# Kernel tuning notes

Measured on AMD Instinct MI355X. Metric: run time of the kernel, lower is better.

Reference implementation:

```python
import jax, jax.numpy as jnp
import numpy as np

EMBED_DIM = 1024
PROJ_DIM = 256


def setup_inputs() -> dict:
    key = jax.random.key(0)
    kx, kq, kk = jax.random.split(key, 3)
    x = jax.random.normal(kx, (8, 4096, EMBED_DIM), dtype=jnp.float32)
    scale = 1.0 / (PROJ_DIM ** 0.5)
    q_proj = jax.random.normal(kq, (EMBED_DIM, PROJ_DIM), dtype=jnp.float32) * scale
    k_proj = jax.random.normal(kk, (EMBED_DIM, PROJ_DIM), dtype=jnp.float32) * scale
    return {"x": x, "q_proj": q_proj, "k_proj": k_proj}


def reference(x, q_proj, k_proj):
    # exp feature maps (FAVOR-style)
    q_prime = jnp.exp(jnp.einsum('bld,de->ble', x, q_proj))  # [B, L, E]
    k_prime = jnp.exp(jnp.einsum('bld,de->ble', x, k_proj))  # [B, L, E]
    # associative KV summary: O(L*E*D)
    kv = jnp.einsum('ble,bld->bed', k_prime, x)               # [B, E, D]
    num = jnp.einsum('ble,bed->bld', q_prime, kv)             # [B, L, D]
    z = 1.0 / (jnp.sum(q_prime, axis=-1, keepdims=True) + 1e-8)
    return num * z
```

## Files before the change

kernel.cpp:

```cpp
#include <hip/hip_runtime.h>


#define EMBED 1024
#define PROJ  256
#define LSEQ  4096
#define BATCH 8

typedef short  bfrag __attribute__((ext_vector_type(8)));
typedef float  f4    __attribute__((ext_vector_type(4)));
typedef unsigned short u16x8 __attribute__((ext_vector_type(8)));
typedef unsigned short u16x4 __attribute__((ext_vector_type(4)));

static __device__ __forceinline__ unsigned short f2bf(float f) {
  unsigned int u = __builtin_bit_cast(unsigned int, f);
  u += 0x7fffu + ((u >> 16) & 1u);
  return (unsigned short)(u >> 16);
}
static __device__ __forceinline__ float bf2f(unsigned short h) {
  unsigned int u = ((unsigned int)h) << 16;
  return __builtin_bit_cast(float, u);
}

static __device__ __forceinline__ void gload_lds16(const void* g, void* l) {
  __builtin_amdgcn_global_load_lds(
      (__attribute__((address_space(1))) void*)(unsigned long long)(g),
      (__attribute__((address_space(3))) void*)(unsigned)(unsigned long long)(l),
      16, 0, 0);
}

static __device__ __forceinline__ void stage_tile(
    const unsigned short* __restrict__ src, int row0, int stride, int k0,
    unsigned short* lds, int wave, int lane) {
#pragma unroll
  for (int j = 0; j < 4; j++) {
    int slot = (wave * 4 + j) * 64 + lane;
    int r = slot >> 3, cp = slot & 7;
    int c = cp ^ (r & 7);
    gload_lds16(src + (size_t)(row0 + r) * stride + k0 + c * 8,
                lds + (wave * 4 + j) * 512);
  }
}

static __device__ __forceinline__ void stage_tile_blk(
    const unsigned short* __restrict__ src, int row0, int ntcols, int k0,
    unsigned short* lds, int wave, int lane) {
#pragma unroll
  for (int j = 0; j < 4; j++) {
    int slot = (wave * 4 + j) * 64 + lane;
    int r = slot >> 3, cp = slot & 7;
    int c = cp ^ (r & 7);
    const unsigned short* blob =
        src + ((((size_t)(row0 >> 6) + (r >> 6)) * ntcols + (k0 >> 6)) << 12);
    gload_lds16(blob + ((r & 63) << 6) + c * 8, lds + (wave * 4 + j) * 512);
  }
}

static __device__ __forceinline__ bfrag read_frag(const unsigned short* lds,
                                                  int row, int chunk) {
  return *(const bfrag*)(lds + ((row << 3) + (chunk ^ (row & 7))) * 8);
}

__global__ __launch_bounds__(256) void cvtb_kernel(
    const float* __restrict__ x, unsigned short* __restrict__ xb) {
  const size_t total = (size_t)BATCH * LSEQ * EMBED;
  size_t i = ((size_t)blockIdx.x * 256 + threadIdx.x) * 8;
  const size_t stride = (size_t)gridDim.x * 256 * 8;
  for (; i < total; i += stride) {
    f4 a = *(const f4*)(x + i);
    f4 b = *(const f4*)(x + i + 4);
    u16x8 h = (u16x8){f2bf(a[0]), f2bf(a[1]), f2bf(a[2]), f2bf(a[3]),
                      f2bf(b[0]), f2bf(b[1]), f2bf(b[2]), f2bf(b[3])};
    *(u16x8*)(xb + i) = h;
  }
}

__global__ __launch_bounds__(256) void cvtw_kernel(
    const float* __restrict__ qw, const float* __restrict__ kw,
    unsigned short* __restrict__ wt) {
  __shared__ unsigned short T[64][72];
  const int tid = threadIdx.x;
  const int n0 = blockIdx.x * 64, k0 = blockIdx.y * 64;
  const float* W = blockIdx.z ? kw : qw;
#pragma unroll
  for (int it = 0; it < 4; it++) {
    int slot = it * 256 + tid;
    int r = slot >> 4, c4 = slot & 15;
    f4 v = *(const f4*)(W + (size_t)(k0 + r) * PROJ + n0 + c4 * 4);
#pragma unroll
    for (int j = 0; j < 4; j++) T[c4 * 4 + j][r] = f2bf(v[j]);
  }
  __syncthreads();
#pragma unroll
  for (int it = 0; it < 2; it++) {
    int slot = it * 256 + tid;
    int n = slot >> 3, ch = slot & 7;
    *(u16x8*)(wt + ((size_t)(blockIdx.z * PROJ + n0 + n)) * EMBED + k0 + ch * 8) =
        *(const u16x8*)&T[n][ch * 8];
  }
}

__global__ __launch_bounds__(256) void proj_kernel(
    const unsigned short* __restrict__ xb, const unsigned short* __restrict__ wt,
    unsigned short* __restrict__ qp, unsigned short* __restrict__ kT) {
  __shared__ union {
    struct { unsigned short A[128 * 64]; unsigned short B[128 * 64]; } t;
    unsigned short T[128 * 136];
  } sm;
  const int tid = threadIdx.x, wave = tid >> 6, lane = tid & 63;
  const int quad = lane >> 4, l16 = lane & 15;
  const int wm = wave >> 1, wn = wave & 1;
  const int n0 = blockIdx.x * 128, m0 = blockIdx.y * 128;

  f4 acc[4][4];
#pragma unroll
  for (int i = 0; i < 4; i++)
#pragma unroll
    for (int j = 0; j < 4; j++) acc[i][j] = (f4){0.f, 0.f, 0.f, 0.f};

  for (int k0 = 0; k0 < EMBED; k0 += 64) {
    stage_tile(xb, m0, EMBED, k0, sm.t.A, wave, lane);
    stage_tile(wt, n0, EMBED, k0, sm.t.B, wave, lane);
    __syncthreads();
#pragma unroll
    for (int ks = 0; ks < 2; ks++) {
      bfrag a[4], bfr[4];
#pragma unroll
      for (int mt = 0; mt < 4; mt++)
        a[mt] = read_frag(sm.t.A, wm * 64 + mt * 16 + l16, ks * 4 + quad);
#pragma unroll
      for (int nt = 0; nt < 4; nt++)
        bfr[nt] = read_frag(sm.t.B, wn * 64 + nt * 16 + l16, ks * 4 + quad);
#pragma unroll
      for (int mt = 0; mt < 4; mt++)
#pragma unroll
        for (int nt = 0; nt < 4; nt++)
          acc[mt][nt] = __builtin_amdgcn_mfma_f32_16x16x32_bf16(
              a[mt], bfr[nt], acc[mt][nt], 0, 0, 0);
    }
    __syncthreads();
  }

  if (n0 < PROJ) {
#pragma unroll
    for (int mt = 0; mt < 4; mt++)
#pragma unroll
      for (int nt = 0; nt < 4; nt++)
#pragma unroll
        for (int r = 0; r < 4; r++)
          sm.T[(wm * 64 + mt * 16 + quad * 4 + r) * 136 + wn * 64 + nt * 16 + l16] =
              f2bf(__expf(acc[mt][nt][r]));
    __syncthreads();
#pragma unroll
    for (int it = 0; it < 8; it++) {
      int slot = it * 256 + tid;
      int row = slot >> 4, ch = slot & 15;
      *(u16x8*)(qp + (size_t)(m0 + row) * PROJ + n0 + ch * 8) =
          *(const u16x8*)&sm.T[row * 136 + ch * 8];
    }
  } else {
#pragma unroll
    for (int mt = 0; mt < 4; mt++)
#pragma unroll
      for (int nt = 0; nt < 4; nt++) {
        u16x4 h;
#pragma unroll
        for (int r = 0; r < 4; r++) h[r] = f2bf(__expf(acc[mt][nt][r]));
        *(u16x4*)&sm.T[(wn * 64 + nt * 16 + l16) * 136 + wm * 64 + mt * 16 + quad * 4] = h;
      }
    __syncthreads();
    const int bb = m0 >> 12, l0w = m0 & 4095, ebase = n0 - PROJ;
#pragma unroll
    for (int it = 0; it < 8; it++) {
      int cid = it * 256 + tid;
      int blobi = cid >> 9, within = cid & 511;
      int er = within >> 3, ch = within & 7;
      int e = (blobi >> 1) * 64 + er, lc = (blobi & 1) * 8 + ch;
      unsigned short* blob =
          kT + ((((size_t)bb * 4 + ((ebase >> 6) + (blobi >> 1))) * 64 +
                 (l0w >> 6) + (blobi & 1)) << 12);
      *(u16x8*)(blob + (er << 6) + ch * 8) = *(const u16x8*)&sm.T[e * 136 + lc * 8];
    }
  }
}

__global__ __launch_bounds__(256) void zinv_kernel(
    const unsigned short* __restrict__ qp, float* __restrict__ zinv) {
  int m = blockIdx.x * 4 + (threadIdx.x >> 6);
  int lane = threadIdx.x & 63;
  u16x4 h = *(const u16x4*)(qp + (size_t)m * PROJ + lane * 4);
  float s = bf2f(h[0]) + bf2f(h[1]) + bf2f(h[2]) + bf2f(h[3]);
#pragma unroll
  for (int off = 32; off; off >>= 1) s += __shfl_xor(s, off);
  if (lane == 0) zinv[m] = 1.0f / (s + 1e-8f);
}

__global__ __launch_bounds__(256) void kv_kernel(
    const unsigned short* __restrict__ kT, const unsigned short* __restrict__ xb,
    float* __restrict__ kvp) {
  __shared__ struct {
    unsigned short A[128 * 64];
    unsigned short B[128 * 64];
    unsigned short T[2][64 * 64];
  } sm;
  const int tid = threadIdx.x, wave = tid >> 6, lane = tid & 63;
  const int quad = lane >> 4, l16 = lane & 15;
  const int wm = wave >> 1, wn = wave & 1;
  const int d0 = blockIdx.x * 128, e0 = blockIdx.y * 128;
  const int b = blockIdx.z & 7, split = blockIdx.z >> 3;
  const unsigned short* As = kT + ((size_t)b * 4 * 64 << 12);
  const unsigned short* xrow = xb + (size_t)b * LSEQ * EMBED;

  f4 acc[4][4];
#pragma unroll
  for (int i = 0; i < 4; i++)
#pragma unroll
    for (int j = 0; j < 4; j++) acc[i][j] = (f4){0.f, 0.f, 0.f, 0.f};

  const int kbase = split * 1024;
  for (int kk = 0; kk < 1024; kk += 64) {
    stage_tile_blk(As, e0, 64, kbase + kk, sm.A, wave, lane);
#pragma unroll
    for (int j = 0; j < 4; j++) {
      int c = (wave * 4 + j) * 64 + lane;
      int r = c >> 4, c16 = c & 15;
      gload_lds16(xrow + (size_t)(kbase + kk + r) * EMBED + d0 + c16 * 8,
                  sm.B + (wave * 4 + j) * 512);
    }
    __syncthreads();
#pragma unroll
    for (int sub = 0; sub < 2; sub++)
#pragma unroll
      for (int it = 0; it < 4; it++) {
        int slot = it * 256 + tid;
        int r = slot >> 4, c4 = slot & 15;
        u16x4 v = *(const u16x4*)(sm.B + r * 128 + sub * 64 + c4 * 4);
        int g = ((r >> 2) ^ c4) << 2;
#pragma unroll
        for (int j2 = 0; j2 < 4; j2++)
          sm.T[sub][(c4 * 4 + j2) * 64 + g + (r & 3)] = v[j2];
      }
    __syncthreads();
#pragma unroll
    for (int it = 0; it < 4; it++) {
      int slot = it * 256 + tid;
      int d = slot >> 3, ch = slot & 7;
      int sub = d >> 6, dl = d & 63, q = dl >> 2;
      u16x4 lo = *(const u16x4*)(sm.T[sub] + dl * 64 + (((2 * ch) ^ q) << 2));
      u16x4 hi = *(const u16x4*)(sm.T[sub] + dl * 64 + (((2 * ch + 1) ^ q) << 2));
      u16x8 o = (u16x8){lo[0], lo[1], lo[2], lo[3], hi[0], hi[1], hi[2], hi[3]};
      *(u16x8*)(sm.B + d * 64 + (ch ^ (d & 7)) * 8) = o;
    }
    __syncthreads();
#pragma unroll
    for (int ks = 0; ks < 2; ks++) {
      bfrag a[4], bfr[4];
#pragma unroll
      for (int mt = 0; mt < 4; mt++)
        a[mt] = read_frag(sm.A, wm * 64 + mt * 16 + l16, ks * 4 + quad);
#pragma unroll
      for (int nt = 0; nt < 4; nt++)
        bfr[nt] = read_frag(sm.B, wn * 64 + nt * 16 + l16, ks * 4 + quad);
#pragma unroll
      for (int mt = 0; mt < 4; mt++)
#pragma unroll
        for (int nt = 0; nt < 4; nt++)
          acc[mt][nt] = __builtin_amdgcn_mfma_f32_16x16x32_bf16(
              a[mt], bfr[nt], acc[mt][nt], 0, 0, 0);
    }
    __syncthreads();
  }

#pragma unroll
  for (int mt = 0; mt < 4; mt++)
#pragma unroll
    for (int nt = 0; nt < 4; nt++)
#pragma unroll
      for (int r = 0; r < 4; r++) {
        int e = e0 + wm * 64 + mt * 16 + quad * 4 + r;
        int d = d0 + wn * 64 + nt * 16 + l16;
        kvp[((size_t)(split * 8 + b) * PROJ + e) * EMBED + d] = acc[mt][nt][r];
      }
}

__global__ __launch_bounds__(256) void kvreduce_kernel(
    const float* __restrict__ kvp, unsigned short* __restrict__ kvT) {
  __shared__ float T[64][68];
  const int tid = threadIdx.x;
  const int d0 = blockIdx.x * 64, e0 = blockIdx.y * 64, b = blockIdx.z;
#pragma unroll
  for (int it = 0; it < 4; it++) {
    int slot = it * 256 + tid;
    int e = slot >> 4, c4 = slot & 15;
    f4 s = (f4){0.f, 0.f, 0.f, 0.f};
#pragma unroll
    for (int sp = 0; sp < 4; sp++)
      s += *(const f4*)(kvp + ((size_t)(sp * 8 + b) * PROJ + e0 + e) * EMBED + d0 + c4 * 4);
#pragma unroll
    for (int j = 0; j < 4; j++) T[c4 * 4 + j][e] = s[j];
  }
  __syncthreads();
#pragma unroll
  for (int it = 0; it < 2; it++) {
    int slot = it * 256 + tid;
    int d = slot >> 3, ch = slot & 7;
    u16x8 h;
#pragma unroll
    for (int j = 0; j < 8; j++) h[j] = f2bf(T[d][ch * 8 + j]);
    *(u16x8*)(kvT + ((size_t)(b * EMBED + d0 + d)) * PROJ + e0 + ch * 8) = h;
  }
}

__global__ __launch_bounds__(256) void out_kernel(
    const unsigned short* __restrict__ qp, const unsigned short* __restrict__ kvT,
    const float* __restrict__ zinv, float* __restrict__ out) {
  __shared__ struct { unsigned short A[128 * 64]; unsigned short B[128 * 64]; } sm;
  __shared__ float zv[128];
  const int tid = threadIdx.x, wave = tid >> 6, lane = tid & 63;
  const int quad = lane >> 4, l16 = lane & 15;
  const int wm = wave >> 1, wn = wave & 1;
  const int d0 = blockIdx.x * 128, l0 = blockIdx.y * 128, b = blockIdx.z;
  const unsigned short* As = qp + (size_t)b * LSEQ * PROJ;
  const unsigned short* Bs = kvT + (size_t)b * EMBED * PROJ;

  if (tid < 128) zv[tid] = zinv[b * LSEQ + l0 + tid];

  f4 acc[4][4];
#pragma unroll
  for (int i = 0; i < 4; i++)
#pragma unroll
    for (int j = 0; j < 4; j++) acc[i][j] = (f4){0.f, 0.f, 0.f, 0.f};

  for (int k0 = 0; k0 < PROJ; k0 += 64) {
    stage_tile(As, l0, PROJ, k0, sm.A, wave, lane);
    stage_tile(Bs, d0, PROJ, k0, sm.B, wave, lane);
    __syncthreads();
#pragma unroll
    for (int ks = 0; ks < 2; ks++) {
      bfrag a[4], bfr[4];
#pragma unroll
      for (int mt = 0; mt < 4; mt++)
        a[mt] = read_frag(sm.A, wm * 64 + mt * 16 + l16, ks * 4 + quad);
#pragma unroll
      for (int nt = 0; nt < 4; nt++)
        bfr[nt] = read_frag(sm.B, wn * 64 + nt * 16 + l16, ks * 4 + quad);
#pragma unroll
      for (int mt = 0; mt < 4; mt++)
#pragma unroll
        for (int nt = 0; nt < 4; nt++)
          acc[mt][nt] = __builtin_amdgcn_mfma_f32_16x16x32_bf16(
              a[mt], bfr[nt], acc[mt][nt], 0, 0, 0);
    }
    __syncthreads();
  }

#pragma unroll
  for (int mt = 0; mt < 4; mt++)
#pragma unroll
    for (int nt = 0; nt < 4; nt++)
#pragma unroll
      for (int r = 0; r < 4; r++) {
        int row = wm * 64 + mt * 16 + quad * 4 + r;
        int d = d0 + wn * 64 + nt * 16 + l16;
        out[((size_t)(b * LSEQ + l0 + row)) * EMBED + d] = acc[mt][nt][r] * zv[row];
      }
}

extern "C" void kernel_launch(void* const* d_in, const int* in_sizes, int n_in,
                              void* d_out, int out_size, void* d_ws, size_t ws_size,
                              hipStream_t stream) {
  const float* x  = (const float*)d_in[0];
  const float* qw = (const float*)d_in[1];
  const float* kw = (const float*)d_in[2];
  float* out = (float*)d_out;

  char* ws = (char*)d_ws;
  unsigned short* xb   = (unsigned short*)(ws);
  float*          kvp  = (float*)(ws + 67108864);
  unsigned short* wt   = (unsigned short*)(ws + 134217728);
  unsigned short* qp   = (unsigned short*)(ws + 135266304);
  unsigned short* kT   = (unsigned short*)(ws + 152043520);
  unsigned short* kvT  = (unsigned short*)(ws + 168820736);
  float*          zinv = (float*)(ws + 173015040);

  cvtb_kernel<<<dim3(2048), 256, 0, stream>>>(x, xb);
  cvtw_kernel<<<dim3(4, 16, 2), 256, 0, stream>>>(qw, kw, wt);
  proj_kernel<<<dim3(4, 256), 256, 0, stream>>>(xb, wt, qp, kT);
  zinv_kernel<<<dim3(8192), 256, 0, stream>>>(qp, zinv);
  kv_kernel<<<dim3(8, 2, 32), 256, 0, stream>>>(kT, xb, kvp);
  kvreduce_kernel<<<dim3(16, 4, 8), 256, 0, stream>>>(kvp, kvT);
  out_kernel<<<dim3(8, 32, 8), 256, 0, stream>>>(qp, kvT, zinv, out);
}
```

Baseline: 367.8 us.

## Double-buffer kv_kernel global loads and fuse the two-pass LDS transpose

Adds double-buffered LDS for the A and raw B tiles so the next tile's global-to-LDS loads are issued before the current tile is computed, with manual vmcnt waits and barriers replacing __syncthreads. Replaces the two-pass transpose through an intermediate buffer with a single-pass swizzled transpose. The swizzle on the raw staging layout is meant to avoid LDS bank conflicts. The aim is to hide global load latency and cut LDS traffic and barriers in the KV accumulation GEMM, at the cost of more LDS per block (possibly lower occupancy) and fragile hand-written waitcnt logic.

```diff
diff --git a/kernel.cpp b/kernel.cpp
--- a/kernel.cpp
+++ b/kernel.cpp
@@ -197,11 +197,9 @@
 __global__ __launch_bounds__(256) void kv_kernel(
     const unsigned short* __restrict__ kT, const unsigned short* __restrict__ xb,
     float* __restrict__ kvp) {
-  __shared__ struct {
-    unsigned short A[128 * 64];
-    unsigned short B[128 * 64];
-    unsigned short T[2][64 * 64];
-  } sm;
+  __shared__ unsigned short sA[2 * 128 * 64];
+  __shared__ unsigned short sBraw[2 * 64 * 128];
+  __shared__ unsigned short sBtr[128 * 64];
   const int tid = threadIdx.x, wave = tid >> 6, lane = tid & 63;
   const int quad = lane >> 4, l16 = lane & 15;
   const int wm = wave >> 1, wn = wave & 1;
@@ -217,49 +215,63 @@
     for (int j = 0; j < 4; j++) acc[i][j] = (f4){0.f, 0.f, 0.f, 0.f};
 
   const int kbase = split * 1024;
-  for (int kk = 0; kk < 1024; kk += 64) {
-    stage_tile_blk(As, e0, 64, kbase + kk, sm.A, wave, lane);
-#pragma unroll
-    for (int j = 0; j < 4; j++) {
-      int c = (wave * 4 + j) * 64 + lane;
-      int r = c >> 4, c16 = c & 15;
-      gload_lds16(xrow + (size_t)(kbase + kk + r) * EMBED + d0 + c16 * 8,
-                  sm.B + (wave * 4 + j) * 512);
-    }
-    __syncthreads();
-#pragma unroll
-    for (int sub = 0; sub < 2; sub++)
-#pragma unroll
-      for (int it = 0; it < 4; it++) {
-        int slot = it * 256 + tid;
-        int r = slot >> 4, c4 = slot & 15;
-        u16x4 v = *(const u16x4*)(sm.B + r * 128 + sub * 64 + c4 * 4);
-        int g = ((r >> 2) ^ c4) << 2;
-#pragma unroll
-        for (int j2 = 0; j2 < 4; j2++)
-          sm.T[sub][(c4 * 4 + j2) * 64 + g + (r & 3)] = v[j2];
+
+#define STAGE_BRAW(K0, DST)                                                   \
+  {                                                                           \
+    _Pragma("unroll") for (int j = 0; j < 4; j++) {                           \
+      int slot = (wave * 4 + j) * 64 + lane;                                  \
+      int r = slot >> 4, c16 = slot & 15;                                     \
+      int cg = c16 ^ ((r >> 2) & 7);                                          \
+      gload_lds16(xrow + (size_t)((K0) + r) * EMBED + d0 + cg * 8,            \
+                  (DST) + (wave * 4 + j) * 512);                              \
+    }                                                                         \
+  }
+
+  stage_tile_blk(As, e0, 64, kbase, sA, wave, lane);
+  STAGE_BRAW(kbase, sBraw);
+
+  for (int t = 0; t < 16; ++t) {
+    unsigned short* Acur = sA + (t & 1) * 8192;
+    const unsigned short* Bcur = sBraw + (t & 1) * 8192;
+    if (t < 15) {
+      stage_tile_blk(As, e0, 64, kbase + (t + 1) * 64, sA + ((t + 1) & 1) * 8192,
+                     wave, lane);
+      STAGE_BRAW(kbase + (t + 1) * 64, sBraw + ((t + 1) & 1) * 8192);
+      asm volatile("s_waitcnt vmcnt(8)" ::: "memory");
+    } else {
+      asm volatile("s_waitcnt vmcnt(0)" ::: "memory");
+    }
+    __builtin_amdgcn_s_barrier();
+    __builtin_amdgcn_sched_barrier(0);
+
+    {
+      const int gl = tid & 15, cd = tid >> 4;
+      const int c = cd ^ (gl & 7);
+      const unsigned short* src = Bcur + gl * 512 + c * 8;
+      u16x8 i0 = *(const u16x8*)(src);
+      u16x8 i1 = *(const u16x8*)(src + 128);
+      u16x8 i2 = *(const u16x8*)(src + 256);
+      u16x8 i3 = *(const u16x8*)(src + 384);
+#pragma unroll
+      for (int k = 0; k < 8; k++) {
+        int d = cd * 8 + k;
+        u16x4 o = (u16x4){i0[k], i1[k], i2[k], i3[k]};
+        *(u16x4*)(sBtr + d * 64 + (((gl >> 1) ^ (d & 7)) << 3) + ((gl & 1) << 2)) = o;
       }
-    __syncthreads();
-#pragma unroll
-    for (int it = 0; it < 4; it++) {
-      int slot = it * 256 + tid;
-      int d = slot >> 3, ch = slot & 7;
-      int sub = d >> 6, dl = d & 63, q = dl >> 2;
-      u16x4 lo = *(const u16x4*)(sm.T[sub] + dl * 64 + (((2 * ch) ^ q) << 2));
-      u16x4 hi = *(const u16x4*)(sm.T[sub] + dl * 64 + (((2 * ch + 1) ^ q) << 2));
-      u16x8 o = (u16x8){lo[0], lo[1], lo[2], lo[3], hi[0], hi[1], hi[2], hi[3]};
-      *(u16x8*)(sm.B + d * 64 + (ch ^ (d & 7)) * 8) = o;
-    }
-    __syncthreads();
+    }
+    asm volatile("s_waitcnt lgkmcnt(0)" ::: "memory");
+    __builtin_amdgcn_s_barrier();
+    __builtin_amdgcn_sched_barrier(0);
+
 #pragma unroll
     for (int ks = 0; ks < 2; ks++) {
       bfrag a[4], bfr[4];
 #pragma unroll
       for (int mt = 0; mt < 4; mt++)
-        a[mt] = read_frag(sm.A, wm * 64 + mt * 16 + l16, ks * 4 + quad);
+        a[mt] = read_frag(Acur, wm * 64 + mt * 16 + l16, ks * 4 + quad);
 #pragma unroll
       for (int nt = 0; nt < 4; nt++)
-        bfr[nt] = read_frag(sm.B, wn * 64 + nt * 16 + l16, ks * 4 + quad);
+        bfr[nt] = read_frag(sBtr, wn * 64 + nt * 16 + l16, ks * 4 + quad);
 #pragma unroll
       for (int mt = 0; mt < 4; mt++)
 #pragma unroll
@@ -267,8 +279,10 @@
           acc[mt][nt] = __builtin_amdgcn_mfma_f32_16x16x32_bf16(
               a[mt], bfr[nt], acc[mt][nt], 0, 0, 0);
     }
-    __syncthreads();
-  }
+    __builtin_amdgcn_s_barrier();
+    __builtin_amdgcn_sched_barrier(0);
+  }
+#undef STAGE_BRAW
 
 #pragma unroll
   for (int mt = 0; mt < 4; mt++)
```

Result: no change. 364.4 us (-0.9%).
